# Performance work log

Measured on AMD Instinct MI355X. Metric: run time of the kernel, lower is better.

The kernel has to match this reference:

```python
import jax, jax.numpy as jnp
import numpy as np

D_MODEL, D_K, D_V, H = 1024, 64, 64, 16

def xnorm(x, gamma):
    # L2 norm over last axis, keepdims; x * gamma / ||x||
    norm = jnp.sqrt(jnp.sum(x * x, axis=-1, keepdims=True))
    return x * gamma / norm

def setup_inputs() -> dict:
    key = jax.random.key(0)
    ks = jax.random.split(key, 12)
    b, n = 4, 8192
    queries = jax.random.normal(ks[0], (b, n, D_MODEL), dtype=jnp.float32)
    keys_ = jax.random.normal(ks[1], (b, n, D_MODEL), dtype=jnp.float32)
    values = jax.random.normal(ks[2], (b, n, D_MODEL), dtype=jnp.float32)
    std = 0.001
    Wq = jax.random.normal(ks[3], (H * D_K, D_MODEL), dtype=jnp.float32) * std
    Wk = jax.random.normal(ks[4], (H * D_K, D_MODEL), dtype=jnp.float32) * std
    Wv = jax.random.normal(ks[5], (H * D_V, D_MODEL), dtype=jnp.float32) * std
    Wo = jax.random.normal(ks[6], (D_MODEL, H * D_V), dtype=jnp.float32) * std
    bq = jnp.zeros((H * D_K,), jnp.float32)
    bk = jnp.zeros((H * D_K,), jnp.float32)
    bv = jnp.zeros((H * D_V,), jnp.float32)
    bo = jnp.zeros((D_MODEL,), jnp.float32)
    gamma = jax.random.normal(ks[7], (1, H, 1, 1), dtype=jnp.float32)
    return {"queries": queries, "keys": keys_, "values": values,
            "Wq": Wq, "bq": bq, "Wk": Wk, "bk": bk, "Wv": Wv, "bv": bv,
            "Wo": Wo, "bo": bo, "gamma": gamma}

def reference(queries, keys, values, Wq, bq, Wk, bk, Wv, bv, Wo, bo, gamma):
    b, nq, _ = queries.shape
    nk = keys.shape[1]
    # projections (torch Linear: x @ W.T + b)
    q = (queries @ Wq.T + bq).reshape(b, nq, H, D_K).transpose(0, 2, 1, 3)  # [b,h,nq,dk]
    k = (keys @ Wk.T + bk).reshape(b, nk, H, D_K).transpose(0, 2, 3, 1)      # [b,h,dk,nk]
    v = (values @ Wv.T + bv).reshape(b, nk, H, D_V).transpose(0, 2, 1, 3)    # [b,h,nk,dv]
    kv = jnp.einsum('bhdn,bhnv->bhdv', k, v)                                  # [b,h,dk,dv]
    kv_n = xnorm(kv, gamma)
    q_n = xnorm(q, gamma)
    out = jnp.einsum('bhnd,bhdv->bhnv', q_n, kv_n)                            # [b,h,nq,dv]
    out = out.transpose(0, 2, 1, 3).reshape(b, nq, H * D_V)
    return out @ Wo.T + bo
```

## Files before the change

### kernel.cpp

```cpp
#include <hip/hip_runtime.h>
#include <stdint.h>

typedef unsigned short ushort_t;
typedef __attribute__((ext_vector_type(4))) float  floatx4;
typedef __attribute__((ext_vector_type(8))) short  shortx8;

__device__ __forceinline__ float bf2f(ushort_t u) {
  union { float f; unsigned int i; } x; x.i = ((unsigned int)u) << 16; return x.f;
}
__device__ __forceinline__ ushort_t f2bf(float f) {
  union { float f; unsigned int i; } x; x.f = f;
  unsigned int r = x.i + 0x7fffu + ((x.i >> 16) & 1u);
  return (ushort_t)(r >> 16);
}

__device__ __forceinline__ void gl_lds16(const ushort_t* g, ushort_t* l) {
  __builtin_amdgcn_global_load_lds(
      (const __attribute__((address_space(1))) void*)g,
      (__attribute__((address_space(3))) void*)l, 16, 0, 0);
}

__global__ __launch_bounds__(256) void cast_f32_bf16(const float* __restrict__ in,
                                                     ushort_t* __restrict__ out, long n) {
  long i = ((long)blockIdx.x * 256 + threadIdx.x) * 8;
  if (i + 8 > n) return;
  floatx4 a = *(const floatx4*)(in + i);
  floatx4 b = *(const floatx4*)(in + i + 4);
  union { shortx8 v; ushort_t h[8]; } u;
  u.h[0] = f2bf(a.x); u.h[1] = f2bf(a.y); u.h[2] = f2bf(a.z); u.h[3] = f2bf(a.w);
  u.h[4] = f2bf(b.x); u.h[5] = f2bf(b.y); u.h[6] = f2bf(b.z); u.h[7] = f2bf(b.w);
  *(shortx8*)(out + i) = u.v;
}

template <int OMODE, bool PBB>
__global__ __launch_bounds__(256, 2) void gemm_bt(const ushort_t* __restrict__ A,
                                                  const ushort_t* __restrict__ B,
                                                  const float* __restrict__ bias,
                                                  const float* __restrict__ gamma,
                                                  void* __restrict__ Cv) {
  constexpr int K = 1024;
  constexpr int N = 1024;
  __shared__ ushort_t As[128 * 32];
  __shared__ ushort_t Bs[128 * 32];

  const int t    = threadIdx.x;
  const int lane = t & 63;
  const int w    = t >> 6;
  const int wm   = w >> 1, wn = w & 1;
  const size_t row0 = (size_t)blockIdx.x * 128;
  const int    col0 = blockIdx.y * 128;
  const size_t boff = PBB ? ((size_t)(blockIdx.x >> 6)) * (size_t)(1024 * 1024) : 0;

  const int sr = t >> 2;
  const int sc = (t & 3) * 8;
  const ushort_t* Ag = A + (row0 + sr) * K + sc;
  const ushort_t* Bg = B + boff + (size_t)(col0 + sr) * K + sc;
  ushort_t* Al = As + t * 8;
  ushort_t* Bl = Bs + t * 8;

  floatx4 acc[4][4] = {};

  const int kg = (lane >> 4) * 8;
  const int fr = lane & 15;

  for (int k0 = 0; k0 < K; k0 += 32) {
    __syncthreads();
    gl_lds16(Ag + k0, Al);
    gl_lds16(Ag + 64 * K + k0, Al + 2048);
    gl_lds16(Bg + k0, Bl);
    gl_lds16(Bg + 64 * K + k0, Bl + 2048);
    __syncthreads();

    shortx8 af[4], bfr[4];
#pragma unroll
    for (int i = 0; i < 4; ++i) {
      af[i]  = *(const shortx8*)&As[(wm * 64 + i * 16 + fr) * 32 + kg];
      bfr[i] = *(const shortx8*)&Bs[(wn * 64 + i * 16 + fr) * 32 + kg];
    }
#pragma unroll
    for (int mt = 0; mt < 4; ++mt)
#pragma unroll
      for (int nt = 0; nt < 4; ++nt)
        acc[mt][nt] = __builtin_amdgcn_mfma_f32_16x16x32_bf16(af[mt], bfr[nt], acc[mt][nt], 0, 0, 0);
  }

  const int cr = (lane >> 4) * 4;
  const int cc = lane & 15;

  float bcol[4];
#pragma unroll
  for (int nt = 0; nt < 4; ++nt) bcol[nt] = bias[col0 + wn * 64 + nt * 16 + cc];
#pragma unroll
  for (int mt = 0; mt < 4; ++mt)
#pragma unroll
    for (int nt = 0; nt < 4; ++nt)
#pragma unroll
      for (int i = 0; i < 4; ++i) acc[mt][nt][i] += bcol[nt];

  if (OMODE == 1) {
    const int h = blockIdx.y * 2 + wn;
    const float g = gamma[h];
#pragma unroll
    for (int mt = 0; mt < 4; ++mt) {
#pragma unroll
      for (int i = 0; i < 4; ++i) {
        float ss = 0.f;
#pragma unroll
        for (int nt = 0; nt < 4; ++nt) { float v = acc[mt][nt][i]; ss += v * v; }
        ss += __shfl_xor(ss, 1);
        ss += __shfl_xor(ss, 2);
        ss += __shfl_xor(ss, 4);
        ss += __shfl_xor(ss, 8);
        const float sc = g * rsqrtf(ss);
#pragma unroll
        for (int nt = 0; nt < 4; ++nt) acc[mt][nt][i] *= sc;
      }
    }
  }

#pragma unroll
  for (int mt = 0; mt < 4; ++mt) {
    size_t r0 = row0 + wm * 64 + mt * 16 + cr;
#pragma unroll
    for (int nt = 0; nt < 4; ++nt) {
      int col = col0 + wn * 64 + nt * 16 + cc;
#pragma unroll
      for (int i = 0; i < 4; ++i) {
        float v = acc[mt][nt][i];
        size_t idx = (r0 + i) * N + col;
        if (OMODE == 2) ((float*)Cv)[idx]    = v;
        else            ((ushort_t*)Cv)[idx] = f2bf(v);
      }
    }
  }
}

__global__ __launch_bounds__(256) void kv_partial(const ushort_t* __restrict__ Kp,
                                                  const ushort_t* __restrict__ Vp,
                                                  float* __restrict__ kvpart) {
  const int bh = blockIdx.x;
  const int h  = bh & 15;
  const long boff = (long)(bh >> 4) * 8192 * 1024;
  const int s = blockIdx.y;
  const int t = threadIdx.x;
  __shared__ float Kl[64 * 64];
  __shared__ float Vl[64 * 64];

  const int d0 = (t >> 4) * 4;
  const int e0 = (t & 15) * 4;
  float acc[4][4] = {};

  for (int c = 0; c < 4; ++c) {
    const int n0 = s * 256 + c * 64;
    __syncthreads();
#pragma unroll
    for (int r = 0; r < 2; ++r) {
      int row = (t >> 3) + 32 * r;
      int seg = (t & 7) * 8;
      union { shortx8 v; ushort_t hh[8]; } uk, uv;
      uk.v = *(const shortx8*)(Kp + boff + (size_t)(n0 + row) * 1024 + h * 64 + seg);
      uv.v = *(const shortx8*)(Vp + boff + (size_t)(n0 + row) * 1024 + h * 64 + seg);
      floatx4 k03 = { bf2f(uk.hh[0]), bf2f(uk.hh[1]), bf2f(uk.hh[2]), bf2f(uk.hh[3]) };
      floatx4 k47 = { bf2f(uk.hh[4]), bf2f(uk.hh[5]), bf2f(uk.hh[6]), bf2f(uk.hh[7]) };
      floatx4 v03 = { bf2f(uv.hh[0]), bf2f(uv.hh[1]), bf2f(uv.hh[2]), bf2f(uv.hh[3]) };
      floatx4 v47 = { bf2f(uv.hh[4]), bf2f(uv.hh[5]), bf2f(uv.hh[6]), bf2f(uv.hh[7]) };
      *(floatx4*)&Kl[row * 64 + seg]     = k03;
      *(floatx4*)&Kl[row * 64 + seg + 4] = k47;
      *(floatx4*)&Vl[row * 64 + seg]     = v03;
      *(floatx4*)&Vl[row * 64 + seg + 4] = v47;
    }
    __syncthreads();
#pragma unroll 8
    for (int nn = 0; nn < 64; ++nn) {
      floatx4 kk = *(const floatx4*)&Kl[nn * 64 + d0];
      floatx4 vv = *(const floatx4*)&Vl[nn * 64 + e0];
#pragma unroll
      for (int i = 0; i < 4; ++i)
#pragma unroll
        for (int j = 0; j < 4; ++j)
          acc[i][j] += kk[i] * vv[j];
    }
  }
  float* dst = kvpart + ((size_t)bh * 32 + s) * 4096;
#pragma unroll
  for (int i = 0; i < 4; ++i) {
    floatx4 row = { acc[i][0], acc[i][1], acc[i][2], acc[i][3] };
    *(floatx4*)&dst[(d0 + i) * 64 + e0] = row;
  }
}

__global__ __launch_bounds__(256) void kv_norm(const float* __restrict__ kvpart,
                                               const float* __restrict__ gamma,
                                               float* __restrict__ kvn) {
  const int bh = blockIdx.x;
  const int t = threadIdx.x;
  const int d  = t >> 2;
  const int e0 = (t & 3) * 16;
  floatx4 v[4] = {};
  for (int s = 0; s < 32; ++s) {
    const float* p = kvpart + ((size_t)bh * 32 + s) * 4096 + d * 64 + e0;
#pragma unroll
    for (int q = 0; q < 4; ++q) v[q] += *(const floatx4*)(p + q * 4);
  }
  float ss = 0.f;
#pragma unroll
  for (int q = 0; q < 4; ++q)
    ss += v[q].x * v[q].x + v[q].y * v[q].y + v[q].z * v[q].z + v[q].w * v[q].w;
  ss += __shfl_xor(ss, 1, 64);
  ss += __shfl_xor(ss, 2, 64);
  float sc = gamma[bh & 15] * rsqrtf(ss);
  float* dst = kvn + (size_t)bh * 4096 + d * 64 + e0;
#pragma unroll
  for (int q = 0; q < 4; ++q) { floatx4 o = v[q] * sc; *(floatx4*)(dst + q * 4) = o; }
}

__global__ __launch_bounds__(256) void w2_kernel(const float* __restrict__ kvn,
                                                 const float* __restrict__ Wo,
                                                 ushort_t* __restrict__ W2T) {
  const int bh = blockIdx.x;
  const int h  = bh & 15;
  const int ot = blockIdx.y;
  const int t  = threadIdx.x;
  __shared__ float kvt[64 * 64];
  __shared__ float wot[64 * 64];
#pragma unroll
  for (int p = 0; p < 4; ++p) {
    int r  = p * 16 + (t >> 4);
    int c4 = (t & 15) * 4;
    floatx4 a = *(const floatx4*)&kvn[(size_t)bh * 4096 + r * 64 + c4];
    floatx4 b = *(const floatx4*)&Wo[(size_t)(ot * 64 + r) * 1024 + h * 64 + c4];
    kvt[(c4 + 0) * 64 + r] = a.x; kvt[(c4 + 1) * 64 + r] = a.y;
    kvt[(c4 + 2) * 64 + r] = a.z; kvt[(c4 + 3) * 64 + r] = a.w;
    wot[(c4 + 0) * 64 + r] = b.x; wot[(c4 + 1) * 64 + r] = b.y;
    wot[(c4 + 2) * 64 + r] = b.z; wot[(c4 + 3) * 64 + r] = b.w;
  }
  __syncthreads();
  const int d0 = (t >> 4) * 4;
  const int o0 = (t & 15) * 4;
  float acc[4][4] = {};
#pragma unroll 8
  for (int e = 0; e < 64; ++e) {
    floatx4 kk = *(const floatx4*)&kvt[e * 64 + d0];
    floatx4 ww = *(const floatx4*)&wot[e * 64 + o0];
#pragma unroll
    for (int i = 0; i < 4; ++i)
#pragma unroll
      for (int j = 0; j < 4; ++j)
        acc[i][j] += kk[i] * ww[j];
  }
  ushort_t* dst = W2T + (size_t)(bh >> 4) * 1024 * 1024;
#pragma unroll
  for (int j = 0; j < 4; ++j)
#pragma unroll
    for (int i = 0; i < 4; ++i)
      dst[(size_t)(ot * 64 + o0 + j) * 1024 + h * 64 + d0 + i] = f2bf(acc[i][j]);
}

extern "C" void kernel_launch(void* const* d_in, const int* in_sizes, int n_in,
                              void* d_out, int out_size, void* d_ws, size_t ws_size,
                              hipStream_t stream) {
  const float* Xq = (const float*)d_in[0];
  const float* Xk = (const float*)d_in[1];
  const float* Xv = (const float*)d_in[2];
  const float* Wq = (const float*)d_in[3];
  const float* bq = (const float*)d_in[4];
  const float* Wk = (const float*)d_in[5];
  const float* bk = (const float*)d_in[6];
  const float* Wv = (const float*)d_in[7];
  const float* bv = (const float*)d_in[8];
  const float* Wo = (const float*)d_in[9];
  const float* bo = (const float*)d_in[10];
  const float* gamma = (const float*)d_in[11];
  float* out = (float*)d_out;

  const long M  = 4L * 8192;
  const long NE = M * 1024;

  char* ws = (char*)d_ws;
  auto alloc = [&](size_t bytes) { char* p = ws; ws += (bytes + 255) & ~255ull; return p; };
  ushort_t* XBF = (ushort_t*)alloc(NE * 2);
  ushort_t* QBF = (ushort_t*)alloc(NE * 2);
  ushort_t* KBF = (ushort_t*)alloc(NE * 2);
  ushort_t* VBF = (ushort_t*)alloc(NE * 2);
  ushort_t* WQB = (ushort_t*)alloc(1024 * 1024 * 2);
  ushort_t* WKB = (ushort_t*)alloc(1024 * 1024 * 2);
  ushort_t* WVB = (ushort_t*)alloc(1024 * 1024 * 2);
  float*    KVP = (float*)alloc((size_t)64 * 32 * 4096 * 4);
  float*    KVN = (float*)alloc((size_t)64 * 4096 * 4);
  ushort_t* W2T = (ushort_t*)alloc((size_t)4 * 1024 * 1024 * 2);

  cast_f32_bf16<<<512, 256, 0, stream>>>(Wq, WQB, 1024 * 1024);
  cast_f32_bf16<<<512, 256, 0, stream>>>(Wk, WKB, 1024 * 1024);
  cast_f32_bf16<<<512, 256, 0, stream>>>(Wv, WVB, 1024 * 1024);

  dim3 ggrid(256, 8);

  cast_f32_bf16<<<16384, 256, 0, stream>>>(Xq, XBF, NE);
  gemm_bt<1, false><<<ggrid, 256, 0, stream>>>(XBF, WQB, bq, gamma, QBF);
  cast_f32_bf16<<<16384, 256, 0, stream>>>(Xk, XBF, NE);
  gemm_bt<0, false><<<ggrid, 256, 0, stream>>>(XBF, WKB, bk, nullptr, KBF);
  cast_f32_bf16<<<16384, 256, 0, stream>>>(Xv, XBF, NE);
  gemm_bt<0, false><<<ggrid, 256, 0, stream>>>(XBF, WVB, bv, nullptr, VBF);

  kv_partial<<<dim3(64, 32), 256, 0, stream>>>(KBF, VBF, KVP);
  kv_norm<<<64, 256, 0, stream>>>(KVP, gamma, KVN);

  w2_kernel<<<dim3(64, 16), 256, 0, stream>>>(KVN, Wo, W2T);

  gemm_bt<2, true><<<ggrid, 256, 0, stream>>>(QBF, W2T, bo, nullptr, out);
}
```

Measured before the change: 859.8 us.

## Rewrite bf16 GEMM as 256x256 tile, double-buffered, swizzled LDS pipeline

```diff
diff --git a/kernel.cpp b/kernel.cpp
--- a/kernel.cpp
+++ b/kernel.cpp
@@ -19,6 +19,9 @@
       (const __attribute__((address_space(1))) void*)g,
       (__attribute__((address_space(3))) void*)l, 16, 0, 0);
 }
+
+#define BARRIER() __builtin_amdgcn_s_barrier()
+#define SCHED0()  __builtin_amdgcn_sched_barrier(0)
 
 __global__ __launch_bounds__(256) void cast_f32_bf16(const float* __restrict__ in,
                                                      ushort_t* __restrict__ out, long n) {
@@ -32,101 +35,173 @@
   *(shortx8*)(out + i) = u.v;
 }
 
+#define MFMA_QUAD(AH, BH, MH, NH)                                              \
+  SCHED0();                                                                    \
+  __builtin_amdgcn_s_setprio(1);                                               \
+  _Pragma("unroll") for (int i_ = 0; i_ < 4; ++i_)                             \
+  _Pragma("unroll") for (int j_ = 0; j_ < 2; ++j_)                             \
+  _Pragma("unroll") for (int s_ = 0; s_ < 2; ++s_)                             \
+    acc[(MH)*4 + i_][(NH)*2 + j_] = __builtin_amdgcn_mfma_f32_16x16x32_bf16(   \
+        AH[i_][s_], BH[j_][s_], acc[(MH)*4 + i_][(NH)*2 + j_], 0, 0, 0);       \
+  __builtin_amdgcn_s_setprio(0);                                               \
+  SCHED0();
+
 template <int OMODE, bool PBB>
-__global__ __launch_bounds__(256, 2) void gemm_bt(const ushort_t* __restrict__ A,
+__global__ __launch_bounds__(512, 2) void gemm_bt(const ushort_t* __restrict__ A,
                                                   const ushort_t* __restrict__ B,
                                                   const float* __restrict__ bias,
                                                   const float* __restrict__ gamma,
                                                   void* __restrict__ Cv) {
-  constexpr int K = 1024;
-  constexpr int N = 1024;
-  __shared__ ushort_t As[128 * 32];
-  __shared__ ushort_t Bs[128 * 32];
+  constexpr int K  = 1024;
+  constexpr int N  = 1024;
+  constexpr int NT = K / 64;
+
+  __shared__ ushort_t Abuf[2][2][8192];
+  __shared__ ushort_t Bbuf[2][2][8192];
 
   const int t    = threadIdx.x;
   const int lane = t & 63;
   const int w    = t >> 6;
-  const int wm   = w >> 1, wn = w & 1;
-  const size_t row0 = (size_t)blockIdx.x * 128;
-  const int    col0 = blockIdx.y * 128;
-  const size_t boff = PBB ? ((size_t)(blockIdx.x >> 6)) * (size_t)(1024 * 1024) : 0;
-
-  const int sr = t >> 2;
-  const int sc = (t & 3) * 8;
-  const ushort_t* Ag = A + (row0 + sr) * K + sc;
-  const ushort_t* Bg = B + boff + (size_t)(col0 + sr) * K + sc;
-  ushort_t* Al = As + t * 8;
-  ushort_t* Bl = Bs + t * 8;
-
-  floatx4 acc[4][4] = {};
-
-  const int kg = (lane >> 4) * 8;
+  const int wm   = w >> 2;
+  const int wn   = w & 3;
+
+  const int bid  = blockIdx.x;
+  const int perm = ((bid & 7) << 6) | (bid >> 3);
+  const int tx   = perm >> 2;
+  const int ty   = perm & 3;
+  const size_t row0 = (size_t)tx * 256;
+  const int    col0 = ty * 256;
+  const size_t boff = PBB ? ((size_t)(tx >> 5)) * (size_t)(1024 * 1024) : 0;
+
+  const int tr  = t >> 3;
+  const int swz = (t & 7) ^ (tr & 7);
+  const ushort_t* Asrc0 = A + (row0 + tr) * K + swz * 8;
+  const ushort_t* Bsrc0 = B + boff + ((size_t)col0 + (size_t)(tr >> 5) * 64 + (tr & 31)) * K + swz * 8;
+
+  auto stageA = [&](int T, int mh) {
+    ushort_t* dst = &Abuf[T & 1][mh][0] + t * 8;
+    const ushort_t* s0 = Asrc0 + (size_t)mh * 64 * K + T * 64;
+    gl_lds16(s0, dst);
+    gl_lds16(s0 + 128 * K, dst + 4096);
+  };
+  auto stageB = [&](int T, int nh) {
+    ushort_t* dst = &Bbuf[T & 1][nh][0] + t * 8;
+    const ushort_t* s0 = Bsrc0 + (size_t)nh * 32 * K + T * 64;
+    gl_lds16(s0, dst);
+    gl_lds16(s0 + 128 * K, dst + 4096);
+  };
+
   const int fr = lane & 15;
-
-  for (int k0 = 0; k0 < K; k0 += 32) {
-    __syncthreads();
-    gl_lds16(Ag + k0, Al);
-    gl_lds16(Ag + 64 * K + k0, Al + 2048);
-    gl_lds16(Bg + k0, Bl);
-    gl_lds16(Bg + 64 * K + k0, Bl + 2048);
-    __syncthreads();
-
-    shortx8 af[4], bfr[4];
-#pragma unroll
-    for (int i = 0; i < 4; ++i) {
-      af[i]  = *(const shortx8*)&As[(wm * 64 + i * 16 + fr) * 32 + kg];
-      bfr[i] = *(const shortx8*)&Bs[(wn * 64 + i * 16 + fr) * 32 + kg];
-    }
-#pragma unroll
-    for (int mt = 0; mt < 4; ++mt)
-#pragma unroll
-      for (int nt = 0; nt < 4; ++nt)
-        acc[mt][nt] = __builtin_amdgcn_mfma_f32_16x16x32_bf16(af[mt], bfr[nt], acc[mt][nt], 0, 0, 0);
-  }
-
-  const int cr = (lane >> 4) * 4;
-  const int cc = lane & 15;
+  const int g4 = lane >> 4;
+  const int q  = fr & 7;
+  int aRd[2], bRd[2];
+#pragma unroll
+  for (int s = 0; s < 2; ++s) {
+    aRd[s] = (wm * 64 + fr) * 128 + (((4 * s + g4) ^ q) * 16);
+    bRd[s] = (wn * 32 + fr) * 128 + (((4 * s + g4) ^ q) * 16);
+  }
+  const char* AbufB = (const char*)&Abuf[0][0][0];
+  const char* BbufB = (const char*)&Bbuf[0][0][0];
+
+  shortx8 a0[4][2], a1[4][2], b0[2][2], b1[2][2];
+  floatx4 acc[8][4] = {};
+
+  auto ldA = [&](shortx8 (&d)[4][2], int slot, int mh) {
+    const char* base = AbufB + slot * 32768 + mh * 16384;
+#pragma unroll
+    for (int i = 0; i < 4; ++i)
+#pragma unroll
+      for (int s = 0; s < 2; ++s)
+        d[i][s] = *(const shortx8*)(base + i * 2048 + aRd[s]);
+  };
+  auto ldB = [&](shortx8 (&d)[2][2], int slot, int nh) {
+    const char* base = BbufB + slot * 32768 + nh * 16384;
+#pragma unroll
+    for (int j = 0; j < 2; ++j)
+#pragma unroll
+      for (int s = 0; s < 2; ++s)
+        d[j][s] = *(const shortx8*)(base + j * 2048 + bRd[s]);
+  };
+
+  stageA(0, 0); stageB(0, 0); stageA(0, 1); stageB(0, 1);
+  stageA(1, 0); stageB(1, 0); stageA(1, 1);
+  asm volatile("s_waitcnt vmcnt(6)" ::: "memory");
+  SCHED0();
+  BARRIER();
+
+#pragma unroll 2
+  for (int T = 0; T < NT; ++T) {
+    const int slot = T & 1;
+    ldA(a0, slot, 0);
+    ldB(b0, slot, 0);
+    if (T + 1 < NT) stageB(T + 1, 1);
+    BARRIER();
+    asm volatile("s_waitcnt lgkmcnt(0)" ::: "memory");
+    MFMA_QUAD(a0, b0, 0, 0);
+    BARRIER();
+    ldB(b1, slot, 1);
+    if (T + 2 < NT) stageA(T + 2, 0);
+    BARRIER();
+    asm volatile("s_waitcnt lgkmcnt(0)" ::: "memory");
+    MFMA_QUAD(a0, b1, 0, 1);
+    BARRIER();
+    ldA(a1, slot, 1);
+    if (T + 2 < NT) stageB(T + 2, 0);
+    BARRIER();
+    asm volatile("s_waitcnt lgkmcnt(0)" ::: "memory");
+    MFMA_QUAD(a1, b1, 1, 1);
+    BARRIER();
+    if (T + 2 < NT) stageA(T + 2, 1);
+    BARRIER();
+    MFMA_QUAD(a1, b0, 1, 0);
+    if (T + 2 < NT)      { asm volatile("s_waitcnt vmcnt(6)" ::: "memory"); }
+    else if (T + 1 < NT) { asm volatile("s_waitcnt vmcnt(0)" ::: "memory"); }
+    SCHED0();
+    BARRIER();
+  }
+
+  const int cr = g4 * 4;
+  const int cc = fr;
 
   float bcol[4];
 #pragma unroll
-  for (int nt = 0; nt < 4; ++nt) bcol[nt] = bias[col0 + wn * 64 + nt * 16 + cc];
-#pragma unroll
-  for (int mt = 0; mt < 4; ++mt)
-#pragma unroll
-    for (int nt = 0; nt < 4; ++nt)
-#pragma unroll
-      for (int i = 0; i < 4; ++i) acc[mt][nt][i] += bcol[nt];
+  for (int j2 = 0; j2 < 4; ++j2) bcol[j2] = bias[col0 + wn * 64 + j2 * 16 + cc];
+#pragma unroll
+  for (int mt = 0; mt < 8; ++mt)
+#pragma unroll
+    for (int j2 = 0; j2 < 4; ++j2)
+#pragma unroll
+      for (int i = 0; i < 4; ++i) acc[mt][j2][i] += bcol[j2];
 
   if (OMODE == 1) {
-    const int h = blockIdx.y * 2 + wn;
-    const float g = gamma[h];
-#pragma unroll
-    for (int mt = 0; mt < 4; ++mt) {
+    const float gm = gamma[ty * 4 + wn];
+#pragma unroll
+    for (int mt = 0; mt < 8; ++mt) {
 #pragma unroll
       for (int i = 0; i < 4; ++i) {
         float ss = 0.f;
 #pragma unroll
-        for (int nt = 0; nt < 4; ++nt) { float v = acc[mt][nt][i]; ss += v * v; }
+        for (int j2 = 0; j2 < 4; ++j2) { float v = acc[mt][j2][i]; ss += v * v; }
         ss += __shfl_xor(ss, 1);
         ss += __shfl_xor(ss, 2);
         ss += __shfl_xor(ss, 4);
         ss += __shfl_xor(ss, 8);
-        const float sc = g * rsqrtf(ss);
-#pragma unroll
-        for (int nt = 0; nt < 4; ++nt) acc[mt][nt][i] *= sc;
+        const float sc = gm * rsqrtf(ss);
+#pragma unroll
+        for (int j2 = 0; j2 < 4; ++j2) acc[mt][j2][i] *= sc;
       }
     }
   }
 
 #pragma unroll
-  for (int mt = 0; mt < 4; ++mt) {
-    size_t r0 = row0 + wm * 64 + mt * 16 + cr;
-#pragma unroll
-    for (int nt = 0; nt < 4; ++nt) {
-      int col = col0 + wn * 64 + nt * 16 + cc;
+  for (int mt = 0; mt < 8; ++mt) {
+    size_t r0 = row0 + wm * 128 + mt * 16 + cr;
+#pragma unroll
+    for (int j2 = 0; j2 < 4; ++j2) {
+      int col = col0 + wn * 64 + j2 * 16 + cc;
 #pragma unroll
       for (int i = 0; i < 4; ++i) {
-        float v = acc[mt][nt][i];
+        float v = acc[mt][j2][i];
         size_t idx = (r0 + i) * N + col;
         if (OMODE == 2) ((float*)Cv)[idx]    = v;
         else            ((ushort_t*)Cv)[idx] = f2bf(v);
@@ -293,19 +368,19 @@
   cast_f32_bf16<<<512, 256, 0, stream>>>(Wk, WKB, 1024 * 1024);
   cast_f32_bf16<<<512, 256, 0, stream>>>(Wv, WVB, 1024 * 1024);
 
-  dim3 ggrid(256, 8);
+  const int ggrid = 512;
 
   cast_f32_bf16<<<16384, 256, 0, stream>>>(Xq, XBF, NE);
-  gemm_bt<1, false><<<ggrid, 256, 0, stream>>>(XBF, WQB, bq, gamma, QBF);
+  gemm_bt<1, false><<<ggrid, 512, 0, stream>>>(XBF, WQB, bq, gamma, QBF);
   cast_f32_bf16<<<16384, 256, 0, stream>>>(Xk, XBF, NE);
-  gemm_bt<0, false><<<ggrid, 256, 0, stream>>>(XBF, WKB, bk, nullptr, KBF);
+  gemm_bt<0, false><<<ggrid, 512, 0, stream>>>(XBF, WKB, bk, nullptr, KBF);
   cast_f32_bf16<<<16384, 256, 0, stream>>>(Xv, XBF, NE);
-  gemm_bt<0, false><<<ggrid, 256, 0, stream>>>(XBF, WVB, bv, nullptr, VBF);
+  gemm_bt<0, false><<<ggrid, 512, 0, stream>>>(XBF, WVB, bv, nullptr, VBF);
 
   kv_partial<<<dim3(64, 32), 256, 0, stream>>>(KBF, VBF, KVP);
   kv_norm<<<64, 256, 0, stream>>>(KVP, gamma, KVN);
 
   w2_kernel<<<dim3(64, 16), 256, 0, stream>>>(KVN, Wo, W2T);
 
-  gemm_bt<2, true><<<ggrid, 256, 0, stream>>>(QBF, W2T, bo, nullptr, out);
-}
+  gemm_bt<2, true><<<ggrid, 512, 0, stream>>>(QBF, W2T, bo, nullptr, out);
+}
```

Measured after the change: 785.9 us. -8.6%, faster.
